# Performance work log

Measured on AMD Instinct MI355X. Metric: run time of the kernel, lower is better.

The kernel has to match this reference:

```python
import jax, jax.numpy as jnp
import numpy as np

B, L, C_IN, D, H, DFF, NL, NC, PH = 32, 512, 16, 512, 8, 2048, 3, 10, 128
DH = D // H


def circ_conv1d(x, w):
    # x: [B, C, S] with circular padding 1 on spatial dim, w: [O, C, 3]
    xp = jnp.concatenate([x[..., -1:], x, x[..., :1]], axis=-1)
    return jax.lax.conv_general_dilated(xp, w, (1,), 'VALID',
                                        dimension_numbers=('NCH', 'OIH', 'NCH'))


def positional_embedding(length, d):
    pos = jnp.arange(length, dtype=jnp.float32)[:, None]
    div = jnp.exp(jnp.arange(0, d, 2, dtype=jnp.float32) * (-np.log(10000.0) / d))
    pe = jnp.zeros((length, d), jnp.float32)
    pe = pe.at[:, 0::2].set(jnp.sin(pos * div))
    pe = pe.at[:, 1::2].set(jnp.cos(pos * div))
    return pe


def layer_norm(x, g, b):
    m = jnp.mean(x, -1, keepdims=True)
    v = jnp.var(x, -1, keepdims=True)
    return (x - m) / jnp.sqrt(v + 1e-5) * g + b


def projector(x, stats, conv_w, w0, b0, w1, b1, w2):
    # x: [B, L, C_IN] (channels = seq_len, spatial = enc_in), stats: [B, 1, C_IN]
    y = circ_conv1d(x, conv_w)                     # [B, 1, C_IN]
    y = jnp.concatenate([y, stats], axis=1)        # [B, 2, C_IN]
    y = y.reshape(x.shape[0], -1)                  # [B, 2*C_IN]
    h = jax.nn.relu(y @ w0.T + b0)
    h = jax.nn.relu(h @ w1.T + b1)
    return h @ w2.T                                # no bias on output


def setup_inputs() -> dict:
    key = jax.random.key(0)
    ks = iter(jax.random.split(key, 64))
    rn = lambda shape, s=0.02: jax.random.normal(next(ks), shape, jnp.float32) * s
    inp = {
        'x_enc': jax.random.normal(next(ks), (B, L, C_IN), jnp.float32),
        'x_mark_enc': jnp.ones((B, L), jnp.float32),
        'tok_w': rn((D, C_IN, 3)),
        'Wq': rn((NL, D, D)), 'bq': jnp.zeros((NL, D)),
        'Wk': rn((NL, D, D)), 'bk': jnp.zeros((NL, D)),
        'Wv': rn((NL, D, D)), 'bv': jnp.zeros((NL, D)),
        'Wo': rn((NL, D, D)), 'bo': jnp.zeros((NL, D)),
        'W1': rn((NL, DFF, D)), 'b1': jnp.zeros((NL, DFF)),
        'W2': rn((NL, D, DFF)), 'b2': jnp.zeros((NL, D)),
        'ln1_g': jnp.ones((NL, D)), 'ln1_b': jnp.zeros((NL, D)),
        'ln2_g': jnp.ones((NL, D)), 'ln2_b': jnp.zeros((NL, D)),
        'norm_g': jnp.ones((D,)), 'norm_b': jnp.zeros((D,)),
        'proj_w': rn((NC, D * L)), 'proj_b': jnp.zeros((NC,)),
        'tau_conv_w': rn((1, L, 3)), 'tau_w0': rn((PH, 2 * C_IN)), 'tau_b0': jnp.zeros((PH,)),
        'tau_w1': rn((PH, PH)), 'tau_b1': jnp.zeros((PH,)), 'tau_w2': rn((1, PH)),
        'del_conv_w': rn((1, L, 3)), 'del_w0': rn((PH, 2 * C_IN)), 'del_b0': jnp.zeros((PH,)),
        'del_w1': rn((PH, PH)), 'del_b1': jnp.zeros((PH,)), 'del_w2': rn((L, PH)),
    }
    return inp


def reference(x_enc, x_mark_enc, tok_w,
              Wq, bq, Wk, bk, Wv, bv, Wo, bo,
              W1, b1, W2, b2, ln1_g, ln1_b, ln2_g, ln2_b,
              norm_g, norm_b, proj_w, proj_b,
              tau_conv_w, tau_w0, tau_b0, tau_w1, tau_b1, tau_w2,
              del_conv_w, del_w0, del_b0, del_w1, del_b1, del_w2):
    # De-stationary statistics (detached in the original)
    x_raw = jax.lax.stop_gradient(x_enc)
    mean_enc = jnp.mean(x_raw, 1, keepdims=True)                 # [B,1,C]
    std_enc = jnp.sqrt(jnp.var(x_raw, 1, keepdims=True) + 1e-5)  # [B,1,C]
    tau = jnp.exp(projector(x_raw, std_enc, tau_conv_w, tau_w0, tau_b0,
                            tau_w1, tau_b1, tau_w2))             # [B,1]
    delta = projector(x_raw, mean_enc, del_conv_w, del_w0, del_b0,
                      del_w1, del_b1, del_w2)                    # [B,L]

    # DataEmbedding: circular token conv + sinusoidal positional encoding
    tok = circ_conv1d(jnp.transpose(x_enc, (0, 2, 1)), tok_w)    # [B,D,L]
    x = jnp.transpose(tok, (0, 2, 1)) + positional_embedding(L, D)[None]

    scale = 1.0 / np.sqrt(DH)
    tau4 = tau.reshape(B, 1, 1, 1)
    delta4 = delta[:, None, None, :]
    for i in range(NL):
        q = (x @ Wq[i].T + bq[i]).reshape(B, L, H, DH)
        k = (x @ Wk[i].T + bk[i]).reshape(B, L, H, DH)
        v = (x @ Wv[i].T + bv[i]).reshape(B, L, H, DH)
        scores = jnp.einsum('blhe,bshe->bhls', q, k) * tau4 + delta4
        A = jax.nn.softmax(scale * scores, axis=-1)
        o = jnp.einsum('bhls,bshd->blhd', A, v).reshape(B, L, D)
        o = o @ Wo[i].T + bo[i]
        x = layer_norm(x + o, ln1_g[i], ln1_b[i])
        y = jax.nn.gelu(x @ W1[i].T + b1[i], approximate=False) @ W2[i].T + b2[i]
        x = layer_norm(x + y, ln2_g[i], ln2_b[i])
    x = layer_norm(x, norm_g, norm_b)

    out = jax.nn.gelu(x, approximate=False)
    out = out * x_mark_enc[..., None]
    out = out.reshape(B, -1) @ proj_w.T + proj_b                 # [B, NC]
    return out
```

## Files before the change

kernel.cpp:

```cpp
#include <hip/hip_runtime.h>
#include <hip/hip_bf16.h>
#include <cstdint>

#define DEVINL __device__ __forceinline__

typedef unsigned short u16;
typedef short bf16x8 __attribute__((ext_vector_type(8)));
typedef float f32x4 __attribute__((ext_vector_type(4)));

DEVINL u16 f2b(float f) {
    union { float f; uint32_t u; } x{f};
    uint32_t r = x.u + 0x7fffu + ((x.u >> 16) & 1u);
    return (u16)(r >> 16);
}
DEVINL float b2f(u16 h) {
    union { uint32_t u; float f; } x{(uint32_t)h << 16};
    return x.f;
}
DEVINL float gelu_exact(float v) {
    return 0.5f * v * (1.0f + erff(v * 0.70710678118654752f));
}
DEVINL void gload_lds16(const void* g, void* l) {
    __builtin_amdgcn_global_load_lds(
        (const __attribute__((address_space(1))) void*)(uintptr_t)g,
        (__attribute__((address_space(3))) void*)(uint32_t)(uintptr_t)l,
        16, 0, 0);
}

__global__ void f2b_kernel(const float* __restrict__ in, u16* __restrict__ out, int n) {
    int i = (blockIdx.x * 256 + threadIdx.x) * 8;
    if (i + 8 <= n) {
        float4 a = *(const float4*)(in + i);
        float4 b = *(const float4*)(in + i + 4);
        u16 t[8] = {f2b(a.x), f2b(a.y), f2b(a.z), f2b(a.w),
                    f2b(b.x), f2b(b.y), f2b(b.z), f2b(b.w)};
        *(uint4*)(out + i) = *(const uint4*)t;
    }
}

__global__ void packb_kernel(const float* __restrict__ bq, const float* __restrict__ bk,
                             const float* __restrict__ bv, float* __restrict__ out) {
    int idx = blockIdx.x * 256 + threadIdx.x;
    if (idx >= 3 * 1536) return;
    int i = idx / 1536, j = idx - i * 1536;
    float v = (j < 512) ? bq[i * 512 + j]
            : (j < 1024) ? bk[i * 512 + j - 512]
                         : bv[i * 512 + j - 1024];
    out[idx] = v;
}

__global__ void pe_kernel(float* __restrict__ pet) {
    int l = blockIdx.x, d2 = threadIdx.x;
    float freq = expf(-(float)(2 * d2) * 0.0179889460390f);
    float ang = (float)l * freq;
    pet[l * 512 + 2 * d2]     = sinf(ang);
    pet[l * 512 + 2 * d2 + 1] = cosf(ang);
}

__global__ void stats_kernel(const float* __restrict__ xe, float* __restrict__ mean,
                             float* __restrict__ stdv) {
    int b = blockIdx.x, ln = threadIdx.x;
    int c = ln & 15, part = ln >> 4;
    float s = 0.f, sq = 0.f;
    for (int l = part; l < 512; l += 4) {
        float x = xe[(size_t)b * 8192 + l * 16 + c];
        s += x; sq += x * x;
    }
    s += __shfl_xor(s, 16);  s += __shfl_xor(s, 32);
    sq += __shfl_xor(sq, 16); sq += __shfl_xor(sq, 32);
    if (part == 0) {
        float m = s * (1.0f / 512.0f);
        mean[b * 16 + c] = m;
        stdv[b * 16 + c] = sqrtf(sq * (1.0f / 512.0f) - m * m + 1e-5f);
    }
}

__global__ __launch_bounds__(128)
void proj_kernel(const float* __restrict__ xe, const float* __restrict__ stats,
                 const float* __restrict__ cw, const float* __restrict__ w0,
                 const float* __restrict__ b0, const float* __restrict__ w1,
                 const float* __restrict__ b1, const float* __restrict__ w2,
                 float* __restrict__ outp, int outn, int do_exp) {
    __shared__ float zl[32], h0l[128], h1l[128], red[2];
    int b = blockIdx.x, tid = threadIdx.x;
    {
        int c = tid >> 3, part = tid & 7;
        float acc = 0.f;
        for (int l = part; l < 512; l += 8) {
            const float* xr = xe + (size_t)b * 8192 + l * 16;
            float w0v = cw[l * 3 + 0], w1v = cw[l * 3 + 1], w2v = cw[l * 3 + 2];
            acc += xr[(c + 15) & 15] * w0v + xr[c] * w1v + xr[(c + 1) & 15] * w2v;
        }
        acc += __shfl_xor(acc, 1); acc += __shfl_xor(acc, 2); acc += __shfl_xor(acc, 4);
        if (part == 0) zl[c] = acc;
        if (tid < 16) zl[16 + tid] = stats[b * 16 + tid];
    }
    __syncthreads();
    {
        float acc = b0[tid];
        #pragma unroll
        for (int i = 0; i < 32; ++i) acc += zl[i] * w0[tid * 32 + i];
        h0l[tid] = fmaxf(acc, 0.0f);
    }
    __syncthreads();
    {
        float acc = b1[tid];
        for (int i = 0; i < 128; ++i) acc += h0l[i] * w1[tid * 128 + i];
        h1l[tid] = fmaxf(acc, 0.0f);
    }
    __syncthreads();
    if (outn == 1) {
        float p = h1l[tid] * w2[tid];
        p += __shfl_xor(p, 1);  p += __shfl_xor(p, 2);  p += __shfl_xor(p, 4);
        p += __shfl_xor(p, 8);  p += __shfl_xor(p, 16); p += __shfl_xor(p, 32);
        if ((tid & 63) == 0) red[tid >> 6] = p;
        __syncthreads();
        if (tid == 0) {
            float v = red[0] + red[1];
            outp[b] = do_exp ? expf(v) : v;
        }
    } else {
        for (int l = tid; l < outn; l += 128) {
            float acc = 0.f;
            for (int i = 0; i < 128; ++i) acc += h1l[i] * w2[l * 128 + i];
            outp[(size_t)b * outn + l] = acc;
        }
    }
}

__global__ __launch_bounds__(256)
void tokconv_kernel(const float* __restrict__ xe, const float* __restrict__ tw,
                    const float* __restrict__ pet,
                    float* __restrict__ xf, u16* __restrict__ xb) {
    __shared__ float xs[34][16];
    int lt = blockIdx.x, b = blockIdx.y, tid = threadIdx.x;
    int l0 = lt * 32;
    for (int idx = tid; idx < 34 * 16; idx += 256) {
        int r = idx >> 4, c = idx & 15;
        int gl = (l0 - 1 + r + 512) & 511;
        xs[r][c] = xe[(size_t)b * 8192 + gl * 16 + c];
    }
    __syncthreads();
    for (int dd = tid; dd < 512; dd += 256) {
        float twr[48];
        #pragma unroll
        for (int i = 0; i < 48; ++i) twr[i] = tw[dd * 48 + i];
        for (int l = 0; l < 32; ++l) {
            float acc = 0.f;
            #pragma unroll
            for (int c = 0; c < 16; ++c) {
                acc += xs[l][c]     * twr[c * 3 + 0];
                acc += xs[l + 1][c] * twr[c * 3 + 1];
                acc += xs[l + 2][c] * twr[c * 3 + 2];
            }
            float vv = acc + pet[(size_t)(l0 + l) * 512 + dd];
            size_t idx = ((size_t)b * 512 + l0 + l) * 512 + dd;
            xf[idx] = vv;
            xb[idx] = f2b(vv);
        }
    }
}

template <int ACT, int OBF>
__global__ __launch_bounds__(256)
void gemm_bt(const u16* __restrict__ A, const u16* __restrict__ B,
             const float* __restrict__ bias, void* __restrict__ Cv,
             int M, int N, int K) {
    __shared__ u16 Al[128 * 32];
    __shared__ u16 Bl[128 * 32];
    const int tid = threadIdx.x, wv = tid >> 6, ln = tid & 63;
    const int m0 = blockIdx.y * 128, n0 = blockIdx.x * 128;
    const int wm = (wv >> 1) * 64, wn = (wv & 1) * 64;
    f32x4 acc[4][4] = {};
    const int r0 = wv * 16 + (ln >> 2);
    const int sl = ln & 3;
    for (int kt = 0; kt < K; kt += 32) {
        __syncthreads();
        #pragma unroll
        for (int c = 0; c < 2; ++c) {
            int row = r0 + c * 64;
            int ssl = sl ^ ((row >> 1) & 3);
            int ldsoff = row * 32 + sl * 8;
            gload_lds16(A + (size_t)(m0 + row) * K + kt + ssl * 8, (char*)Al + ldsoff * 2);
            gload_lds16(B + (size_t)(n0 + row) * K + kt + ssl * 8, (char*)Bl + ldsoff * 2);
        }
        __syncthreads();
        bf16x8 af[4], bfr[4];
        #pragma unroll
        for (int i = 0; i < 4; ++i) {
            int row = wm + i * 16 + (ln & 15);
            int slot = (ln >> 4) ^ ((row >> 1) & 3);
            af[i] = *(const bf16x8*)(Al + row * 32 + slot * 8);
        }
        #pragma unroll
        for (int j = 0; j < 4; ++j) {
            int row = wn + j * 16 + (ln & 15);
            int slot = (ln >> 4) ^ ((row >> 1) & 3);
            bfr[j] = *(const bf16x8*)(Bl + row * 32 + slot * 8);
        }
        #pragma unroll
        for (int i = 0; i < 4; ++i)
            #pragma unroll
            for (int j = 0; j < 4; ++j)
                acc[i][j] = __builtin_amdgcn_mfma_f32_16x16x32_bf16(af[i], bfr[j], acc[i][j], 0, 0, 0);
    }
    #pragma unroll
    for (int j = 0; j < 4; ++j) {
        int col = n0 + wn + j * 16 + (ln & 15);
        float bv = bias[col];
        #pragma unroll
        for (int i = 0; i < 4; ++i) {
            int rbase = m0 + wm + i * 16 + (ln >> 4) * 4;
            #pragma unroll
            for (int r = 0; r < 4; ++r) {
                float v = acc[i][j][r] + bv;
                if (ACT == 1) v = gelu_exact(v);
                size_t idx = (size_t)(rbase + r) * N + col;
                if (OBF) ((u16*)Cv)[idx] = f2b(v);
                else     ((float*)Cv)[idx] = v;
            }
        }
    }
}

__global__ __launch_bounds__(512)
void attn2_kernel(const u16* __restrict__ qkv, const float* __restrict__ tau,
                  const float* __restrict__ delta, u16* __restrict__ o) {
    __shared__ u16 KL[64 * 64];
    __shared__ u16 VT[64 * 72];
    __shared__ u16 PL[8][32 * 64];
    const int tid = threadIdx.x, w = tid >> 6, ln = tid & 63;
    const int lo = ln & 15, hi = ln >> 4;
    const int qh = blockIdx.x, h = blockIdx.y, b = blockIdx.z;
    const size_t qrow0 = (size_t)b * 512;
    const u16* qp = qkv;
    const u16* kp = qkv + 512;
    const u16* vp = qkv + 1024;
    const int hofs = h * 64;
    const float ts = tau[b] * 0.125f;
    u16* Pw = (u16*)PL[w];
    const int q0 = qh * 256 + w * 32;

    bf16x8 qa[2][2];
    #pragma unroll
    for (int i = 0; i < 2; ++i)
        #pragma unroll
        for (int ks = 0; ks < 2; ++ks)
            qa[i][ks] = *(const bf16x8*)(qp + (qrow0 + q0 + i * 16 + lo) * 1536 + hofs + ks * 32 + hi * 8);

    float m_run[2] = {-1e30f, -1e30f};
    float l_run[2] = {0.f, 0.f};
    f32x4 oacc[2][4] = {};

    const int vsl = tid & 7, vsr = tid >> 3;
    uint4 vreg = *(const uint4*)(vp + (qrow0 + vsr) * 1536 + hofs + vsl * 8);

    for (int nt = 0; nt < 8; ++nt) {
        __syncthreads();
        {
            int s = tid >> 3, j = tid & 7;
            int jl = j ^ (s & 7);
            gload_lds16(kp + (qrow0 + nt * 64 + s) * 1536 + hofs + jl * 8,
                        (char*)KL + tid * 16);
        }
        {
            u16 tmp[8]; *(uint4*)tmp = vreg;
            #pragma unroll
            for (int e = 0; e < 8; ++e) {
                int d = vsl * 8 + e;
                int byt = d * 144 + (((vsr >> 3) ^ vsl) << 4) + (vsr & 7) * 2;
                *(u16*)((char*)VT + byt) = tmp[e];
            }
        }
        if (nt < 7)
            vreg = *(const uint4*)(vp + (qrow0 + (nt + 1) * 64 + vsr) * 1536 + hofs + vsl * 8);
        __syncthreads();

        f32x4 sacc[2][4] = {};
        #pragma unroll
        for (int ks = 0; ks < 2; ++ks) {
            #pragma unroll
            for (int jn = 0; jn < 4; ++jn) {
                int s = jn * 16 + lo;
                int phys = (ks * 4 + hi) ^ (s & 7);
                bf16x8 kb = *(const bf16x8*)((const char*)KL + s * 128 + phys * 16);
                #pragma unroll
                for (int i = 0; i < 2; ++i)
                    sacc[i][jn] = __builtin_amdgcn_mfma_f32_16x16x32_bf16(kb, qa[i][ks], sacc[i][jn], 0, 0, 0);
            }
        }
        float tmax[2] = {-1e30f, -1e30f};
        #pragma unroll
        for (int jn = 0; jn < 4; ++jn) {
            float4 dv4 = *(const float4*)(delta + b * 512 + nt * 64 + jn * 16 + hi * 4);
            float dv[4] = {dv4.x, dv4.y, dv4.z, dv4.w};
            #pragma unroll
            for (int i = 0; i < 2; ++i)
                #pragma unroll
                for (int r = 0; r < 4; ++r) {
                    float v = sacc[i][jn][r] * ts + dv[r] * 0.125f;
                    sacc[i][jn][r] = v;
                    tmax[i] = fmaxf(tmax[i], v);
                }
        }
        #pragma unroll
        for (int i = 0; i < 2; ++i) {
            tmax[i] = fmaxf(tmax[i], __shfl_xor(tmax[i], 16));
            tmax[i] = fmaxf(tmax[i], __shfl_xor(tmax[i], 32));
            float mnew = fmaxf(m_run[i], tmax[i]);
            float fac = __expf(m_run[i] - mnew);
            m_run[i] = mnew;
            l_run[i] *= fac;
            #pragma unroll
            for (int jd = 0; jd < 4; ++jd)
                #pragma unroll
                for (int r = 0; r < 4; ++r) oacc[i][jd][r] *= fac;
        }
        #pragma unroll
        for (int i = 0; i < 2; ++i) {
            float ls = 0.f;
            #pragma unroll
            for (int jn = 0; jn < 4; ++jn) {
                float p0 = __expf(sacc[i][jn][0] - m_run[i]);
                float p1 = __expf(sacc[i][jn][1] - m_run[i]);
                float p2 = __expf(sacc[i][jn][2] - m_run[i]);
                float p3 = __expf(sacc[i][jn][3] - m_run[i]);
                ls += (p0 + p1) + (p2 + p3);
                uint2 pk;
                pk.x = (uint32_t)f2b(p0) | ((uint32_t)f2b(p1) << 16);
                pk.y = (uint32_t)f2b(p2) | ((uint32_t)f2b(p3) << 16);
                int q = i * 16 + lo;
                int ls16 = jn * 2 + (hi >> 1);
                int byt = q * 128 + (((ls16 ^ (q & 7)) << 4)) + (hi & 1) * 8;
                *(uint2*)((char*)Pw + byt) = pk;
            }
            ls += __shfl_xor(ls, 16);
            ls += __shfl_xor(ls, 32);
            l_run[i] += ls;
        }
        #pragma unroll
        for (int ks2 = 0; ks2 < 2; ++ks2) {
            bf16x8 pa[2];
            #pragma unroll
            for (int i = 0; i < 2; ++i) {
                int q = i * 16 + lo;
                int phys = (ks2 * 4 + hi) ^ (q & 7);
                pa[i] = *(const bf16x8*)((const char*)Pw + q * 128 + phys * 16);
            }
            #pragma unroll
            for (int jd = 0; jd < 4; ++jd) {
                int d = jd * 16 + lo;
                int cs = (ks2 * 4 + hi) ^ ((d >> 3) & 7);
                bf16x8 vb = *(const bf16x8*)((const char*)VT + d * 144 + cs * 16);
                #pragma unroll
                for (int i = 0; i < 2; ++i)
                    oacc[i][jd] = __builtin_amdgcn_mfma_f32_16x16x32_bf16(vb, pa[i], oacc[i][jd], 0, 0, 0);
            }
        }
    }
    #pragma unroll
    for (int i = 0; i < 2; ++i) {
        float inv = 1.0f / l_run[i];
        #pragma unroll
        for (int jd = 0; jd < 4; ++jd) {
            u16 t4[4];
            #pragma unroll
            for (int r = 0; r < 4; ++r) t4[r] = f2b(oacc[i][jd][r] * inv);
            size_t row = qrow0 + q0 + i * 16 + lo;
            *(uint2*)(o + row * 512 + hofs + jd * 16 + hi * 4) = *(const uint2*)t4;
        }
    }
}

__global__ __launch_bounds__(256)
void ln_kernel(const float* __restrict__ xin, const float* __restrict__ res,
               const float* __restrict__ g, const float* __restrict__ bta,
               float* __restrict__ xout, u16* __restrict__ xbf) {
    const int row = blockIdx.x * 4 + (threadIdx.x >> 6);
    const int ln = threadIdx.x & 63;
    const float* xr = xin + (size_t)row * 512;
    const float* rr = res + (size_t)row * 512;
    float4 a = *(const float4*)(xr + ln * 4);
    float4 c = *(const float4*)(xr + 256 + ln * 4);
    float4 ra = *(const float4*)(rr + ln * 4);
    float4 rc = *(const float4*)(rr + 256 + ln * 4);
    a.x += ra.x; a.y += ra.y; a.z += ra.z; a.w += ra.w;
    c.x += rc.x; c.y += rc.y; c.z += rc.z; c.w += rc.w;
    float s = a.x + a.y + a.z + a.w + c.x + c.y + c.z + c.w;
    float sq = a.x*a.x + a.y*a.y + a.z*a.z + a.w*a.w + c.x*c.x + c.y*c.y + c.z*c.z + c.w*c.w;
    #pragma unroll
    for (int m = 1; m < 64; m <<= 1) { s += __shfl_xor(s, m); sq += __shfl_xor(sq, m); }
    float mean = s * 0.001953125f;
    float var = sq * 0.001953125f - mean * mean;
    float rstd = rsqrtf(var + 1e-5f);
    float4 g0 = *(const float4*)(g + ln * 4);
    float4 g1 = *(const float4*)(g + 256 + ln * 4);
    float4 b0 = *(const float4*)(bta + ln * 4);
    float4 b1 = *(const float4*)(bta + 256 + ln * 4);
    float4 o0, o1;
    o0.x = (a.x - mean) * rstd * g0.x + b0.x;
    o0.y = (a.y - mean) * rstd * g0.y + b0.y;
    o0.z = (a.z - mean) * rstd * g0.z + b0.z;
    o0.w = (a.w - mean) * rstd * g0.w + b0.w;
    o1.x = (c.x - mean) * rstd * g1.x + b1.x;
    o1.y = (c.y - mean) * rstd * g1.y + b1.y;
    o1.z = (c.z - mean) * rstd * g1.z + b1.z;
    o1.w = (c.w - mean) * rstd * g1.w + b1.w;
    *(float4*)(xout + (size_t)row * 512 + ln * 4) = o0;
    *(float4*)(xout + (size_t)row * 512 + 256 + ln * 4) = o1;
    u16 t0[4] = {f2b(o0.x), f2b(o0.y), f2b(o0.z), f2b(o0.w)};
    u16 t1[4] = {f2b(o1.x), f2b(o1.y), f2b(o1.z), f2b(o1.w)};
    *(uint2*)(xbf + (size_t)row * 512 + ln * 4) = *(const uint2*)t0;
    *(uint2*)(xbf + (size_t)row * 512 + 256 + ln * 4) = *(const uint2*)t1;
}

__global__ __launch_bounds__(256)
void lngelu_kernel(const float* __restrict__ xin, const float* __restrict__ g,
                   const float* __restrict__ bta, const float* __restrict__ mark,
                   u16* __restrict__ outb) {
    const int row = blockIdx.x * 4 + (threadIdx.x >> 6);
    const int ln = threadIdx.x & 63;
    const float* xr = xin + (size_t)row * 512;
    float4 a = *(const float4*)(xr + ln * 4);
    float4 c = *(const float4*)(xr + 256 + ln * 4);
    float s = a.x + a.y + a.z + a.w + c.x + c.y + c.z + c.w;
    float sq = a.x*a.x + a.y*a.y + a.z*a.z + a.w*a.w + c.x*c.x + c.y*c.y + c.z*c.z + c.w*c.w;
    #pragma unroll
    for (int m = 1; m < 64; m <<= 1) { s += __shfl_xor(s, m); sq += __shfl_xor(sq, m); }
    float mean = s * 0.001953125f;
    float var = sq * 0.001953125f - mean * mean;
    float rstd = rsqrtf(var + 1e-5f);
    float mk = mark[row];
    float4 g0 = *(const float4*)(g + ln * 4);
    float4 g1 = *(const float4*)(g + 256 + ln * 4);
    float4 b0 = *(const float4*)(bta + ln * 4);
    float4 b1 = *(const float4*)(bta + 256 + ln * 4);
    float v0 = gelu_exact((a.x - mean) * rstd * g0.x + b0.x) * mk;
    float v1 = gelu_exact((a.y - mean) * rstd * g0.y + b0.y) * mk;
    float v2 = gelu_exact((a.z - mean) * rstd * g0.z + b0.z) * mk;
    float v3 = gelu_exact((a.w - mean) * rstd * g0.w + b0.w) * mk;
    float v4 = gelu_exact((c.x - mean) * rstd * g1.x + b1.x) * mk;
    float v5 = gelu_exact((c.y - mean) * rstd * g1.y + b1.y) * mk;
    float v6 = gelu_exact((c.z - mean) * rstd * g1.z + b1.z) * mk;
    float v7 = gelu_exact((c.w - mean) * rstd * g1.w + b1.w) * mk;
    u16 t0[4] = {f2b(v0), f2b(v1), f2b(v2), f2b(v3)};
    u16 t1[4] = {f2b(v4), f2b(v5), f2b(v6), f2b(v7)};
    *(uint2*)(outb + (size_t)row * 512 + ln * 4) = *(const uint2*)t0;
    *(uint2*)(outb + (size_t)row * 512 + 256 + ln * 4) = *(const uint2*)t1;
}

__global__ __launch_bounds__(256)
void fproj_kernel(const u16* __restrict__ gb, const u16* __restrict__ pw,
                  const float* __restrict__ pb, float* __restrict__ out) {
    __shared__ float red[32][4];
    int n = blockIdx.x, ks = blockIdx.y, tid = threadIdx.x;
    float acc[32];
    #pragma unroll
    for (int m = 0; m < 32; ++m) acc[m] = 0.f;
    for (int j = 0; j < 8; ++j) {
        size_t k0 = (size_t)ks * 16384 + j * 2048 + tid * 8;
        bf16x8 w8 = *(const bf16x8*)(pw + (size_t)n * 262144 + k0);
        float wf[8];
        #pragma unroll
        for (int e = 0; e < 8; ++e) wf[e] = b2f((u16)w8[e]);
        #pragma unroll
        for (int m = 0; m < 32; ++m) {
            bf16x8 g8 = *(const bf16x8*)(gb + (size_t)m * 262144 + k0);
            float a = acc[m];
            #pragma unroll
            for (int e = 0; e < 8; ++e) a += b2f((u16)g8[e]) * wf[e];
            acc[m] = a;
        }
    }
    int w = tid >> 6;
    #pragma unroll
    for (int m = 0; m < 32; ++m) {
        float s = acc[m];
        s += __shfl_xor(s, 1);  s += __shfl_xor(s, 2);  s += __shfl_xor(s, 4);
        s += __shfl_xor(s, 8);  s += __shfl_xor(s, 16); s += __shfl_xor(s, 32);
        if ((tid & 63) == 0) red[m][w] = s;
    }
    __syncthreads();
    if (tid < 32) {
        int m = tid;
        float s = red[m][0] + red[m][1] + red[m][2] + red[m][3];
        if (ks == 0) s += pb[n];
        atomicAdd(&out[m * 10 + n], s);
    }
}

extern "C" void kernel_launch(void* const* d_in, const int* in_sizes, int n_in,
                              void* d_out, int out_size, void* d_ws, size_t ws_size,
                              hipStream_t stream) {
    const float* x_enc  = (const float*)d_in[0];
    const float* x_mark = (const float*)d_in[1];
    const float* tok_w  = (const float*)d_in[2];
    const float* Wq = (const float*)d_in[3];   const float* bq = (const float*)d_in[4];
    const float* Wk = (const float*)d_in[5];   const float* bk = (const float*)d_in[6];
    const float* Wv = (const float*)d_in[7];   const float* bv = (const float*)d_in[8];
    const float* Wo = (const float*)d_in[9];   const float* bo = (const float*)d_in[10];
    const float* W1 = (const float*)d_in[11];  const float* b1 = (const float*)d_in[12];
    const float* W2 = (const float*)d_in[13];  const float* b2 = (const float*)d_in[14];
    const float* ln1_g = (const float*)d_in[15]; const float* ln1_b = (const float*)d_in[16];
    const float* ln2_g = (const float*)d_in[17]; const float* ln2_b = (const float*)d_in[18];
    const float* norm_g = (const float*)d_in[19]; const float* norm_b = (const float*)d_in[20];
    const float* proj_w = (const float*)d_in[21]; const float* proj_b = (const float*)d_in[22];
    const float* tau_cw = (const float*)d_in[23];
    const float* tau_w0 = (const float*)d_in[24]; const float* tau_b0 = (const float*)d_in[25];
    const float* tau_w1 = (const float*)d_in[26]; const float* tau_b1 = (const float*)d_in[27];
    const float* tau_w2 = (const float*)d_in[28];
    const float* del_cw = (const float*)d_in[29];
    const float* del_w0 = (const float*)d_in[30]; const float* del_b0 = (const float*)d_in[31];
    const float* del_w1 = (const float*)d_in[32]; const float* del_b1 = (const float*)d_in[33];
    const float* del_w2 = (const float*)d_in[34];
    float* out = (float*)d_out;

    char* ws = (char*)d_ws;
    size_t off = 0;
    auto alloc = [&](size_t bytes) -> void* {
        void* p = ws + off;
        off += (bytes + 255) & ~(size_t)255;
        return p;
    };
    u16* wqkvb = (u16*)alloc((size_t)3 * 786432 * 2);
    u16* wob = (u16*)alloc(786432 * 2);
    u16* w1b = (u16*)alloc(3145728 * 2);
    u16* w2b = (u16*)alloc(3145728 * 2);
    u16* pwb = (u16*)alloc(2621440 * 2);
    float* bqkvb = (float*)alloc(3 * 1536 * 4);
    float* petab = (float*)alloc((size_t)262144 * 4);
    float* meanb = (float*)alloc(512 * 4);
    float* stdb  = (float*)alloc(512 * 4);
    float* taub  = (float*)alloc(32 * 4);
    float* delb  = (float*)alloc(16384 * 4);
    float* xf = (float*)alloc((size_t)8388608 * 4);
    u16*  xb  = (u16*)alloc((size_t)8388608 * 2);
    float* sf = (float*)alloc((size_t)8388608 * 4);
    u16* qkvb = (u16*)alloc((size_t)16384 * 1536 * 2);
    u16* ob   = (u16*)alloc((size_t)8388608 * 2);
    u16* hb   = qkvb;
    u16* gbuf = qkvb;

    auto cvt = [&](const float* src, u16* dst, int n) {
        f2b_kernel<<<dim3((n + 2047) / 2048), dim3(256), 0, stream>>>(src, dst, n);
    };
    for (int i = 0; i < 3; ++i) {
        cvt(Wq + (size_t)i * 262144, wqkvb + (size_t)i * 786432 + 0,      262144);
        cvt(Wk + (size_t)i * 262144, wqkvb + (size_t)i * 786432 + 262144, 262144);
        cvt(Wv + (size_t)i * 262144, wqkvb + (size_t)i * 786432 + 524288, 262144);
    }
    cvt(Wo, wob, 786432);
    cvt(W1, w1b, 3145728); cvt(W2, w2b, 3145728);
    cvt(proj_w, pwb, 2621440);
    packb_kernel<<<dim3(18), dim3(256), 0, stream>>>(bq, bk, bv, bqkvb);
    pe_kernel<<<dim3(512), dim3(256), 0, stream>>>(petab);

    stats_kernel<<<dim3(32), dim3(64), 0, stream>>>(x_enc, meanb, stdb);
    proj_kernel<<<dim3(32), dim3(128), 0, stream>>>(x_enc, stdb, tau_cw, tau_w0, tau_b0,
                                                    tau_w1, tau_b1, tau_w2, taub, 1, 1);
    proj_kernel<<<dim3(32), dim3(128), 0, stream>>>(x_enc, meanb, del_cw, del_w0, del_b0,
                                                    del_w1, del_b1, del_w2, delb, 512, 0);
    tokconv_kernel<<<dim3(16, 32), dim3(256), 0, stream>>>(x_enc, tok_w, petab, xf, xb);

    for (int i = 0; i < 3; ++i) {
        const u16* wqkv_i = wqkvb + (size_t)i * 786432;
        const u16* wo_i = wob + (size_t)i * 262144;
        const u16* w1_i = w1b + (size_t)i * 1048576;
        const u16* w2_i = w2b + (size_t)i * 1048576;
        gemm_bt<0, 1><<<dim3(12, 128), dim3(256), 0, stream>>>(xb, wqkv_i, bqkvb + i * 1536, qkvb, 16384, 1536, 512);
        attn2_kernel<<<dim3(2, 8, 32), dim3(512), 0, stream>>>(qkvb, taub, delb, ob);
        gemm_bt<0, 0><<<dim3(4, 128), dim3(256), 0, stream>>>(ob, wo_i, bo + i * 512, sf, 16384, 512, 512);
        ln_kernel<<<dim3(4096), dim3(256), 0, stream>>>(xf, sf, ln1_g + i * 512, ln1_b + i * 512, xf, xb);
        gemm_bt<1, 1><<<dim3(16, 128), dim3(256), 0, stream>>>(xb, w1_i, b1 + i * 2048, hb, 16384, 2048, 512);
        gemm_bt<0, 0><<<dim3(4, 128), dim3(256), 0, stream>>>(hb, w2_i, b2 + i * 512, sf, 16384, 512, 2048);
        ln_kernel<<<dim3(4096), dim3(256), 0, stream>>>(xf, sf, ln2_g + i * 512, ln2_b + i * 512, xf, xb);
    }

    lngelu_kernel<<<dim3(4096), dim3(256), 0, stream>>>(xf, norm_g, norm_b, x_mark, gbuf);
    hipMemsetAsync(d_out, 0, (size_t)out_size * 4, stream);
    fproj_kernel<<<dim3(10, 16), dim3(256), 0, stream>>>(gbuf, pwb, proj_b, out);
}
```

Before: 1.029 ms.

## Double-buffer GEMM LDS tiles and vectorize epilogue stores through shared memory

```diff
diff --git a/kernel.cpp b/kernel.cpp
--- a/kernel.cpp
+++ b/kernel.cpp
@@ -166,58 +166,79 @@
 void gemm_bt(const u16* __restrict__ A, const u16* __restrict__ B,
              const float* __restrict__ bias, void* __restrict__ Cv,
              int M, int N, int K) {
-    __shared__ u16 Al[128 * 32];
-    __shared__ u16 Bl[128 * 32];
+    __shared__ u16 smem[2][2][128 * 32];
     const int tid = threadIdx.x, wv = tid >> 6, ln = tid & 63;
     const int m0 = blockIdx.y * 128, n0 = blockIdx.x * 128;
     const int wm = (wv >> 1) * 64, wn = (wv & 1) * 64;
+    const int lo = ln & 15, hi = ln >> 4;
     f32x4 acc[4][4] = {};
     const int r0 = wv * 16 + (ln >> 2);
     const int sl = ln & 3;
-    for (int kt = 0; kt < K; kt += 32) {
-        __syncthreads();
+
+    auto stage = [&](int buf, int kt) {
         #pragma unroll
         for (int c = 0; c < 2; ++c) {
             int row = r0 + c * 64;
             int ssl = sl ^ ((row >> 1) & 3);
             int ldsoff = row * 32 + sl * 8;
-            gload_lds16(A + (size_t)(m0 + row) * K + kt + ssl * 8, (char*)Al + ldsoff * 2);
-            gload_lds16(B + (size_t)(n0 + row) * K + kt + ssl * 8, (char*)Bl + ldsoff * 2);
-        }
-        __syncthreads();
+            gload_lds16(A + (size_t)(m0 + row) * K + kt + ssl * 8, (char*)smem[buf][0] + ldsoff * 2);
+            gload_lds16(B + (size_t)(n0 + row) * K + kt + ssl * 8, (char*)smem[buf][1] + ldsoff * 2);
+        }
+    };
+
+    stage(0, 0);
+    __syncthreads();
+    int cur = 0;
+    const int nt = K >> 5;
+    for (int t = 0; t < nt; ++t) {
+        if (t + 1 < nt) stage(cur ^ 1, (t + 1) * 32);
         bf16x8 af[4], bfr[4];
         #pragma unroll
         for (int i = 0; i < 4; ++i) {
-            int row = wm + i * 16 + (ln & 15);
-            int slot = (ln >> 4) ^ ((row >> 1) & 3);
-            af[i] = *(const bf16x8*)(Al + row * 32 + slot * 8);
+            int row = wm + i * 16 + lo;
+            int slot = hi ^ ((row >> 1) & 3);
+            af[i] = *(const bf16x8*)(smem[cur][0] + row * 32 + slot * 8);
         }
         #pragma unroll
         for (int j = 0; j < 4; ++j) {
-            int row = wn + j * 16 + (ln & 15);
-            int slot = (ln >> 4) ^ ((row >> 1) & 3);
-            bfr[j] = *(const bf16x8*)(Bl + row * 32 + slot * 8);
+            int row = wn + j * 16 + lo;
+            int slot = hi ^ ((row >> 1) & 3);
+            bfr[j] = *(const bf16x8*)(smem[cur][1] + row * 32 + slot * 8);
         }
         #pragma unroll
         for (int i = 0; i < 4; ++i)
             #pragma unroll
             for (int j = 0; j < 4; ++j)
                 acc[i][j] = __builtin_amdgcn_mfma_f32_16x16x32_bf16(af[i], bfr[j], acc[i][j], 0, 0, 0);
-    }
+        __syncthreads();
+        cur ^= 1;
+    }
+
+    float* ep = (float*)smem + wv * (16 * 68);
     #pragma unroll
-    for (int j = 0; j < 4; ++j) {
-        int col = n0 + wn + j * 16 + (ln & 15);
-        float bv = bias[col];
-        #pragma unroll
-        for (int i = 0; i < 4; ++i) {
-            int rbase = m0 + wm + i * 16 + (ln >> 4) * 4;
+    for (int i = 0; i < 4; ++i) {
+        #pragma unroll
+        for (int j = 0; j < 4; ++j) {
+            int col = n0 + wn + j * 16 + lo;
+            float bv = bias[col];
             #pragma unroll
             for (int r = 0; r < 4; ++r) {
                 float v = acc[i][j][r] + bv;
                 if (ACT == 1) v = gelu_exact(v);
-                size_t idx = (size_t)(rbase + r) * N + col;
-                if (OBF) ((u16*)Cv)[idx] = f2b(v);
-                else     ((float*)Cv)[idx] = v;
+                ep[(hi * 4 + r) * 68 + j * 16 + lo] = v;
+            }
+        }
+        #pragma unroll
+        for (int pp = 0; pp < 4; ++pp) {
+            int rl = pp * 4 + hi;
+            float4 vv = *(const float4*)(ep + rl * 68 + lo * 4);
+            size_t row = (size_t)(m0 + wm + i * 16 + rl);
+            int col = n0 + wn + lo * 4;
+            if (OBF) {
+                u16 t4[4] = {f2b(vv.x), f2b(vv.y), f2b(vv.z), f2b(vv.w)};
+                *(uint2*)((u16*)Cv + row * N + col) = *(const uint2*)t4;
+            } else {
+                *(float4*)((float*)Cv + row * N + col) = vv;
             }
         }
     }
```

New measurement: 967.2 us. 6.0% less time.
